# Kernel optimization log

Hardware: AMD Instinct MI355X
Metric: run time of the kernel (lower is better)

The kernel has to match this reference:

```python
import jax, jax.numpy as jnp
import numpy as np

B, S, H, D = 32, 127, 4, 64
HD = H * D
SCALE = 1.0 / np.sqrt(D).astype(np.float32)
NEG = -100000.0


def _remove_mask_keep(seq_len):
    # For q>=3, rows are grouped in 2-row blocks starting at i=3,5,...;
    # each block may only attend (among k>=3) to its own two columns.
    q = jnp.arange(seq_len)[:, None]
    k = jnp.arange(seq_len)[None, :]
    blk = 3 + 2 * ((q - 3) // 2)
    return (q < 3) | (k < 3) | ((k >= blk) & (k < blk + 2))  # [S, S] bool


def setup_inputs() -> dict:
    rng = jax.random.key(0)
    ks = jax.random.split(rng, 16)
    n = lambda k, shape: jax.random.normal(k, shape, dtype=jnp.float32)
    w = 1.0 / np.sqrt(HD).astype(np.float32)
    return {
        "query": n(ks[0], (B, S, HD)),
        "key": n(ks[1], (B, S, HD)),
        "value": n(ks[2], (B, S, HD)),
        "graph": jax.random.randint(ks[3], (B, S, S), 0, 2, dtype=jnp.int32),
        "edge_key": n(ks[4], (B, S, S, D)),
        "edge_value": n(ks[5], (B, S, S, D)),
        "edge_query": n(ks[6], (B, S, S, D)),
        "Wq": n(ks[7], (HD, HD)) * w, "bq": jnp.zeros((HD,), jnp.float32),
        "Wk": n(ks[8], (HD, HD)) * w, "bk": jnp.zeros((HD,), jnp.float32),
        "Wv": n(ks[9], (HD, HD)) * w, "bv": jnp.zeros((HD,), jnp.float32),
        "Wo": n(ks[10], (HD, HD)) * w, "bo": jnp.zeros((HD,), jnp.float32),
    }


def reference(query, key, value, graph, edge_key, edge_value, edge_query,
              Wq, bq, Wk, bk, Wv, bv, Wo, bo):
    b, s, _ = query.shape
    q = (query @ Wq.T + bq).reshape(b, s, H, D)
    k = (key @ Wk.T + bk).reshape(b, s, H, D)
    v = (value @ Wv.T + bv).reshape(b, s, H, D)

    scores = (
        jnp.einsum('bqhd,bkhd->bhqk', q, k)
        + jnp.einsum('bqhd,bqkd->bhqk', q, edge_key)
        + jnp.einsum('bkqd,bkhd->bhqk', edge_query, k)
        + jnp.einsum('bkqd,bqkd->bqk', edge_query, edge_key)[:, None]
    ) * SCALE

    mask = (graph != 0)[:, None, :, :] & _remove_mask_keep(s)[None, None]
    scores = jnp.where(mask, scores, NEG)
    attn = jax.nn.softmax(scores, axis=-1)  # dropout p=0 -> identity

    x = (jnp.einsum('bhqk,bkhd->bqhd', attn, v)
         + jnp.einsum('bhqk,bqkd->bqhd', attn, edge_value)).reshape(b, s, HD)
    return x @ Wo.T + bo
```

## Files before the change

### kernel.cpp

```cpp
#include <hip/hip_runtime.h>
#include <hip/hip_bf16.h>

#define S_LEN 127
#define NB    32
#define HDIM  256
#define DH    64
#define SCALE_F 0.125f

typedef __bf16 bf16x8 __attribute__((ext_vector_type(8)));
typedef __bf16 bf16x4 __attribute__((ext_vector_type(4)));
typedef float  f32x4  __attribute__((ext_vector_type(4)));

#define NTOK  4064
#define NW4   16384

__device__ __forceinline__ float4 b2f4(bf16x4 v) {
  return make_float4((float)v[0], (float)v[1], (float)v[2], (float)v[3]);
}

__global__ __launch_bounds__(256) void convert_w(
    const float* __restrict__ Wq, const float* __restrict__ Wk,
    const float* __restrict__ Wv, const float* __restrict__ Wo,
    __bf16* __restrict__ Wqb, __bf16* __restrict__ Wkb,
    __bf16* __restrict__ Wvb, __bf16* __restrict__ Wob)
{
  size_t t = (size_t)blockIdx.x * 256 + threadIdx.x;
  const float* src; __bf16* dst;
  if (t < NW4)                 { src = Wq; dst = Wqb; }
  else if ((t -= NW4) < NW4)   { src = Wk; dst = Wkb; }
  else if ((t -= NW4) < NW4)   { src = Wv; dst = Wvb; }
  else { t -= NW4;               src = Wo; dst = Wob; }
  const float4 x = ((const float4*)src)[t];
  bf16x4 r;
  r[0] = (__bf16)x.x; r[1] = (__bf16)x.y; r[2] = (__bf16)x.z; r[3] = (__bf16)x.w;
  ((bf16x4*)dst)[t] = r;
}

__global__ __launch_bounds__(256) void gemm_qkv(
    const float* __restrict__ q_in, const float* __restrict__ k_in,
    const float* __restrict__ v_in,
    const __bf16* __restrict__ Wqb, const float* __restrict__ bq,
    const __bf16* __restrict__ Wkb, const float* __restrict__ bk,
    const __bf16* __restrict__ Wvb, const float* __restrict__ bv,
    __bf16* __restrict__ qpb, __bf16* __restrict__ kpb, __bf16* __restrict__ vpb)
{
  const int tile = blockIdx.x;
  const float* A; const __bf16* W; const float* bias; __bf16* o;
  if (blockIdx.y == 0)      { A = q_in; W = Wqb; bias = bq; o = qpb; }
  else if (blockIdx.y == 1) { A = k_in; W = Wkb; bias = bk; o = kpb; }
  else                      { A = v_in; W = Wvb; bias = bv; o = vpb; }

  __shared__ __bf16 sA[32][264];
  const int row0 = tile * 32;

#pragma unroll
  for (int j = 0; j < 8; ++j) {
    const int f = threadIdx.x + j * 256;
    const int rr = f >> 6, c4 = f & 63;
    const float4 x = *(const float4*)(A + (size_t)(row0 + rr) * HDIM + c4 * 4);
    __bf16* d = &sA[rr][c4 * 4];
    d[0] = (__bf16)x.x; d[1] = (__bf16)x.y; d[2] = (__bf16)x.z; d[3] = (__bf16)x.w;
  }
  __syncthreads();

  const int w    = threadIdx.x >> 6;
  const int lane = threadIdx.x & 63;
  const int r    = lane & 15;
  const int ksl  = (lane >> 4) << 3;
  const int wc   = w * 64;

  const __bf16* Wb = W + (size_t)(wc + r) * HDIM + ksl;
  f32x4 acc[2][4] = {};

  bf16x8 cw[4];
#pragma unroll
  for (int ni = 0; ni < 4; ++ni)
    cw[ni] = *(const bf16x8*)(Wb + (size_t)ni * 16 * HDIM);
#pragma unroll
  for (int kb = 0; kb < 8; ++kb) {
    bf16x8 nw[4];
    if (kb < 7) {
#pragma unroll
      for (int ni = 0; ni < 4; ++ni)
        nw[ni] = *(const bf16x8*)(Wb + (size_t)ni * 16 * HDIM + (kb + 1) * 32);
    }
    const bf16x8 a0 = *(const bf16x8*)&sA[r][kb * 32 + ksl];
    const bf16x8 a1 = *(const bf16x8*)&sA[16 + r][kb * 32 + ksl];
#pragma unroll
    for (int ni = 0; ni < 4; ++ni) {
      acc[0][ni] = __builtin_amdgcn_mfma_f32_16x16x32_bf16(a0, cw[ni], acc[0][ni], 0, 0, 0);
      acc[1][ni] = __builtin_amdgcn_mfma_f32_16x16x32_bf16(a1, cw[ni], acc[1][ni], 0, 0, 0);
    }
    if (kb < 7) {
#pragma unroll
      for (int ni = 0; ni < 4; ++ni) cw[ni] = nw[ni];
    }
  }
  const int crow = (lane >> 4) * 4;
  const int ccol = lane & 15;
#pragma unroll
  for (int mi = 0; mi < 2; ++mi)
#pragma unroll
    for (int ni = 0; ni < 4; ++ni) {
      const int oc = wc + ni * 16 + ccol;
      const float bv = bias[oc];
#pragma unroll
      for (int rg = 0; rg < 4; ++rg)
        o[(size_t)(row0 + mi * 16 + crow + rg) * HDIM + oc] =
            (__bf16)(acc[mi][ni][rg] + bv);
    }
}

__global__ __launch_bounds__(256) void gemm_o(
    const __bf16* __restrict__ A, const __bf16* __restrict__ W,
    const float* __restrict__ bias, float* __restrict__ out)
{
  const int w = threadIdx.x >> 6;
  const int tile = blockIdx.x * 4 + w;
  if (tile >= 127) return;
  const int row0 = tile * 32, col0 = blockIdx.y * 32;
  const int lane = threadIdx.x & 63;
  const int r  = lane & 15;
  const int ks = (lane >> 4) << 3;
  const __bf16* Ab = A + (size_t)(row0 + r) * HDIM + ks;
  const __bf16* Wb = W + (size_t)(col0 + r) * HDIM + ks;
  f32x4 acc[2][2] = {};

  bf16x8 ca[2], cw[2];
  ca[0] = *(const bf16x8*)Ab;
  ca[1] = *(const bf16x8*)(Ab + (size_t)16 * HDIM);
  cw[0] = *(const bf16x8*)Wb;
  cw[1] = *(const bf16x8*)(Wb + (size_t)16 * HDIM);
#pragma unroll
  for (int kb = 0; kb < 8; ++kb) {
    bf16x8 na[2], nw[2];
    if (kb < 7) {
      const int off = (kb + 1) * 32;
      na[0] = *(const bf16x8*)(Ab + off);
      na[1] = *(const bf16x8*)(Ab + (size_t)16 * HDIM + off);
      nw[0] = *(const bf16x8*)(Wb + off);
      nw[1] = *(const bf16x8*)(Wb + (size_t)16 * HDIM + off);
    }
#pragma unroll
    for (int mi = 0; mi < 2; ++mi)
#pragma unroll
      for (int ni = 0; ni < 2; ++ni)
        acc[mi][ni] = __builtin_amdgcn_mfma_f32_16x16x32_bf16(
            ca[mi], cw[ni], acc[mi][ni], 0, 0, 0);
    if (kb < 7) {
      ca[0] = na[0]; ca[1] = na[1];
      cw[0] = nw[0]; cw[1] = nw[1];
    }
  }
  const int crow = (lane >> 4) * 4;
  const int ccol = lane & 15;
#pragma unroll
  for (int mi = 0; mi < 2; ++mi)
#pragma unroll
    for (int ni = 0; ni < 2; ++ni) {
      const int oc = col0 + ni * 16 + ccol;
      const float bv = bias[oc];
#pragma unroll
      for (int rg = 0; rg < 4; ++rg)
        out[(size_t)(row0 + mi * 16 + crow + rg) * HDIM + oc] = acc[mi][ni][rg] + bv;
    }
}

__global__ __launch_bounds__(256) void attn_kernel(
    const __bf16* __restrict__ qpb, const __bf16* __restrict__ kpb,
    const __bf16* __restrict__ vpb, const int* __restrict__ graph,
    const float* __restrict__ ekt, const float* __restrict__ evt,
    const float* __restrict__ eqt, __bf16* __restrict__ xpb)
{
  int b, q;
  {
    const int bx = blockIdx.x;
    if (bx < 96) { b = bx / 3; q = bx % 3; }
    else { const int rr = bx - 96; b = rr / 124; q = 3 + rr % 124; }
  }
  const int t = threadIdx.x;
  const int w = t >> 6;
  const int l = t & 63;
  const int ll = l & 15;
  const int g  = l >> 4;

  __shared__ int   s_list[S_LEN];
  __shared__ float s_attn[4][S_LEN];
  __shared__ int   s_cnt[2];

  bool valid = false;
  const int k0 = w * 64 + l;
  if (w < 2 && k0 < S_LEN) {
    const int gr = graph[((size_t)b * S_LEN + q) * S_LEN + k0];
    bool keep;
    if (q < 3 || k0 < 3) keep = true;
    else {
      const int blk = 3 + 2 * ((q - 3) >> 1);
      keep = (k0 >= blk) & (k0 < blk + 2);
    }
    valid = (gr != 0) && keep;
  }
  const unsigned long long bal = __ballot(valid);
  if (w < 2 && l == 0) s_cnt[w] = (int)__popcll(bal);
  __syncthreads();
  int n = s_cnt[0] + s_cnt[1];
  if (valid) {
    const int pos = (int)__popcll(bal & ((1ull << l) - 1ull)) + (w ? s_cnt[0] : 0);
    s_list[pos] = k0;
  }
  __syncthreads();

  if (n == 0) {
    if (t < S_LEN) {
      s_list[t] = t;
      const float u = 1.0f / 127.0f;
      s_attn[0][t] = u; s_attn[1][t] = u; s_attn[2][t] = u; s_attn[3][t] = u;
    }
    n = S_LEN;
  } else {
    const __bf16* qrow = qpb + ((size_t)b * S_LEN + q) * HDIM;
    float4 q4[4];
#pragma unroll
    for (int h = 0; h < 4; ++h)
      q4[h] = b2f4(*(const bf16x4*)(qrow + h * 64 + ll * 4));
    const float* eqb2 = eqt + ((size_t)b * S_LEN * S_LEN + q) * DH;
    const float* ekb2 = ekt + ((size_t)(b * S_LEN + q)) * S_LEN * DH;
    const __bf16* kpbb = kpb + (size_t)b * S_LEN * HDIM;
    const int myi = w * 4 + g;

    float4 ceq, cek;
    bf16x4 ck0, ck1, ck2, ck3;
    if (myi < n) {
      const int kk = s_list[myi];
      ceq = *(const float4*)(eqb2 + (size_t)kk * (S_LEN * DH) + ll * 4);
      cek = *(const float4*)(ekb2 + kk * DH + ll * 4);
      const __bf16* kr = kpbb + (size_t)kk * HDIM + ll * 4;
      ck0 = *(const bf16x4*)(kr);
      ck1 = *(const bf16x4*)(kr + 64);
      ck2 = *(const bf16x4*)(kr + 128);
      ck3 = *(const bf16x4*)(kr + 192);
    }
    for (int i0 = 0; i0 < n; i0 += 16) {
      const int i = i0 + myi;
      float4 neq, nek;
      bf16x4 nk0, nk1, nk2, nk3;
      const int j = i + 16;
      if (j < n) {
        const int kk = s_list[j];
        neq = *(const float4*)(eqb2 + (size_t)kk * (S_LEN * DH) + ll * 4);
        nek = *(const float4*)(ekb2 + kk * DH + ll * 4);
        const __bf16* kr = kpbb + (size_t)kk * HDIM + ll * 4;
        nk0 = *(const bf16x4*)(kr);
        nk1 = *(const bf16x4*)(kr + 64);
        nk2 = *(const bf16x4*)(kr + 128);
        nk3 = *(const bf16x4*)(kr + 192);
      }
      float p0 = 0.f, p1 = 0.f, p2 = 0.f, p3 = 0.f;
      if (i < n) {
        const float4 k0f = b2f4(ck0), k1f = b2f4(ck1),
                     k2f = b2f4(ck2), k3f = b2f4(ck3);
        p0 = (q4[0].x+ceq.x)*(k0f.x+cek.x) + (q4[0].y+ceq.y)*(k0f.y+cek.y)
           + (q4[0].z+ceq.z)*(k0f.z+cek.z) + (q4[0].w+ceq.w)*(k0f.w+cek.w);
        p1 = (q4[1].x+ceq.x)*(k1f.x+cek.x) + (q4[1].y+ceq.y)*(k1f.y+cek.y)
           + (q4[1].z+ceq.z)*(k1f.z+cek.z) + (q4[1].w+ceq.w)*(k1f.w+cek.w);
        p2 = (q4[2].x+ceq.x)*(k2f.x+cek.x) + (q4[2].y+ceq.y)*(k2f.y+cek.y)
           + (q4[2].z+ceq.z)*(k2f.z+cek.z) + (q4[2].w+ceq.w)*(k2f.w+cek.w);
        p3 = (q4[3].x+ceq.x)*(k3f.x+cek.x) + (q4[3].y+ceq.y)*(k3f.y+cek.y)
           + (q4[3].z+ceq.z)*(k3f.z+cek.z) + (q4[3].w+ceq.w)*(k3f.w+cek.w);
      }
#pragma unroll
      for (int off = 1; off < 16; off <<= 1) {
        p0 += __shfl_xor(p0, off, 64);
        p1 += __shfl_xor(p1, off, 64);
        p2 += __shfl_xor(p2, off, 64);
        p3 += __shfl_xor(p3, off, 64);
      }
      if (i < n && ll < 4) {
        const float s = (ll == 0) ? p0 : (ll == 1) ? p1 : (ll == 2) ? p2 : p3;
        s_attn[ll][i] = s * SCALE_F;
      }
      ceq = neq; cek = nek;
      ck0 = nk0; ck1 = nk1; ck2 = nk2; ck3 = nk3;
    }
    __syncthreads();

    {
      const float v0 = (l < n) ? s_attn[w][l] : -INFINITY;
      const float v1 = (64 + l < n) ? s_attn[w][64 + l] : -INFINITY;
      float mx = fmaxf(v0, v1);
#pragma unroll
      for (int off = 32; off; off >>= 1) mx = fmaxf(mx, __shfl_xor(mx, off, 64));
      const float e0 = (l < n) ? expf(v0 - mx) : 0.f;
      const float e1 = (64 + l < n) ? expf(v1 - mx) : 0.f;
      float sm = e0 + e1;
#pragma unroll
      for (int off = 32; off; off >>= 1) sm += __shfl_xor(sm, off, 64);
      const float inv = 1.0f / sm;
      if (l < n) s_attn[w][l] = e0 * inv;
      if (64 + l < n) s_attn[w][64 + l] = e1 * inv;
    }
  }
  __syncthreads();

  {
    const float* evb2 = evt + ((size_t)(b * S_LEN + q)) * S_LEN * DH;
    const __bf16* vbp = vpb + (size_t)b * S_LEN * HDIM + w * DH + ll * 4;
    float ax = 0.f, ay = 0.f, az = 0.f, aw2 = 0.f;

    int i = g;
    float a = 0.f; bf16x4 v4; float4 e4;
    if (i < n) {
      const int kk = s_list[i];
      a = s_attn[w][i];
      v4 = *(const bf16x4*)(vbp + (size_t)kk * HDIM);
      e4 = *(const float4*)(evb2 + kk * DH + ll * 4);
    }
    while (i < n) {
      const int j = i + 4;
      float a2 = 0.f; bf16x4 v42; float4 e42;
      if (j < n) {
        const int kk = s_list[j];
        a2 = s_attn[w][j];
        v42 = *(const bf16x4*)(vbp + (size_t)kk * HDIM);
        e42 = *(const float4*)(evb2 + kk * DH + ll * 4);
      }
      const float4 vf = b2f4(v4);
      ax  += a * (vf.x + e4.x);
      ay  += a * (vf.y + e4.y);
      az  += a * (vf.z + e4.z);
      aw2 += a * (vf.w + e4.w);
      i = j; a = a2; v4 = v42; e4 = e42;
    }
#pragma unroll
    for (int off = 16; off < 64; off <<= 1) {
      ax  += __shfl_xor(ax, off, 64);
      ay  += __shfl_xor(ay, off, 64);
      az  += __shfl_xor(az, off, 64);
      aw2 += __shfl_xor(aw2, off, 64);
    }
    if (g == 0) {
      bf16x4 rr;
      rr[0] = (__bf16)ax; rr[1] = (__bf16)ay;
      rr[2] = (__bf16)az; rr[3] = (__bf16)aw2;
      *(bf16x4*)(xpb + ((size_t)b * S_LEN + q) * HDIM + w * 64 + ll * 4) = rr;
    }
  }
}

extern "C" void kernel_launch(void* const* d_in, const int* in_sizes, int n_in,
                              void* d_out, int out_size, void* d_ws, size_t ws_size,
                              hipStream_t stream) {
  const float* query = (const float*)d_in[0];
  const float* key   = (const float*)d_in[1];
  const float* value = (const float*)d_in[2];
  const int*   graph = (const int*)d_in[3];
  const float* ekt   = (const float*)d_in[4];
  const float* evt   = (const float*)d_in[5];
  const float* eqt   = (const float*)d_in[6];
  const float* Wq = (const float*)d_in[7];  const float* bq = (const float*)d_in[8];
  const float* Wk = (const float*)d_in[9];  const float* bk = (const float*)d_in[10];
  const float* Wv = (const float*)d_in[11]; const float* bv = (const float*)d_in[12];
  const float* Wo = (const float*)d_in[13]; const float* bo = (const float*)d_in[14];
  float* out = (float*)d_out;

  const size_t NE = (size_t)NTOK * HDIM;
  char* p = (char*)d_ws;
  __bf16* qpb = (__bf16*)p;         p += NE * 2;
  __bf16* kpb = (__bf16*)p;         p += NE * 2;
  __bf16* vpb = (__bf16*)p;         p += NE * 2;
  __bf16* xpb = (__bf16*)p;         p += NE * 2;
  __bf16* Wqb = (__bf16*)p;         p += (size_t)HDIM * HDIM * 2;
  __bf16* Wkb = (__bf16*)p;         p += (size_t)HDIM * HDIM * 2;
  __bf16* Wvb = (__bf16*)p;         p += (size_t)HDIM * HDIM * 2;
  __bf16* Wob = (__bf16*)p;

  convert_w<<<dim3(256), 256, 0, stream>>>(Wq, Wk, Wv, Wo, Wqb, Wkb, Wvb, Wob);
  gemm_qkv<<<dim3(127, 3), 256, 0, stream>>>(query, key, value,
                                             Wqb, bq, Wkb, bk, Wvb, bv,
                                             qpb, kpb, vpb);
  attn_kernel<<<dim3(NB * S_LEN), 256, 0, stream>>>(qpb, kpb, vpb, graph,
                                                    ekt, evt, eqt, xpb);
  gemm_o<<<dim3(32, 8), 256, 0, stream>>>(xpb, Wob, bo, out);
}
```

Baseline: 51.99 us.

## Fuse output projection into attention kernel with 4 tokens per block

Merges the attention kernel and the output-projection GEMM into one kernel. Each 1024-thread block handles four (batch, query) items, keeps their attention outputs in LDS, and multiplies them by Wo with MFMA, padding the 16-row tile with zeros. This drops the separate gemm_o launch and the global round trip of the intermediate x tensor. In exchange, every block rereads the whole 256x256 Wo, only 4 of 16 MFMA rows are useful, and the larger blocks with more barriers can lower occupancy.

After: 84.91 us. 63.3% more time.

```diff
diff --git a/kernel.cpp b/kernel.cpp
--- a/kernel.cpp
+++ b/kernel.cpp
@@ -111,82 +111,37 @@
     }
 }
 
-__global__ __launch_bounds__(256) void gemm_o(
-    const __bf16* __restrict__ A, const __bf16* __restrict__ W,
-    const float* __restrict__ bias, float* __restrict__ out)
-{
-  const int w = threadIdx.x >> 6;
-  const int tile = blockIdx.x * 4 + w;
-  if (tile >= 127) return;
-  const int row0 = tile * 32, col0 = blockIdx.y * 32;
-  const int lane = threadIdx.x & 63;
-  const int r  = lane & 15;
-  const int ks = (lane >> 4) << 3;
-  const __bf16* Ab = A + (size_t)(row0 + r) * HDIM + ks;
-  const __bf16* Wb = W + (size_t)(col0 + r) * HDIM + ks;
-  f32x4 acc[2][2] = {};
-
-  bf16x8 ca[2], cw[2];
-  ca[0] = *(const bf16x8*)Ab;
-  ca[1] = *(const bf16x8*)(Ab + (size_t)16 * HDIM);
-  cw[0] = *(const bf16x8*)Wb;
-  cw[1] = *(const bf16x8*)(Wb + (size_t)16 * HDIM);
-#pragma unroll
-  for (int kb = 0; kb < 8; ++kb) {
-    bf16x8 na[2], nw[2];
-    if (kb < 7) {
-      const int off = (kb + 1) * 32;
-      na[0] = *(const bf16x8*)(Ab + off);
-      na[1] = *(const bf16x8*)(Ab + (size_t)16 * HDIM + off);
-      nw[0] = *(const bf16x8*)(Wb + off);
-      nw[1] = *(const bf16x8*)(Wb + (size_t)16 * HDIM + off);
-    }
-#pragma unroll
-    for (int mi = 0; mi < 2; ++mi)
-#pragma unroll
-      for (int ni = 0; ni < 2; ++ni)
-        acc[mi][ni] = __builtin_amdgcn_mfma_f32_16x16x32_bf16(
-            ca[mi], cw[ni], acc[mi][ni], 0, 0, 0);
-    if (kb < 7) {
-      ca[0] = na[0]; ca[1] = na[1];
-      cw[0] = nw[0]; cw[1] = nw[1];
-    }
-  }
-  const int crow = (lane >> 4) * 4;
-  const int ccol = lane & 15;
-#pragma unroll
-  for (int mi = 0; mi < 2; ++mi)
-#pragma unroll
-    for (int ni = 0; ni < 2; ++ni) {
-      const int oc = col0 + ni * 16 + ccol;
-      const float bv = bias[oc];
-#pragma unroll
-      for (int rg = 0; rg < 4; ++rg)
-        out[(size_t)(row0 + mi * 16 + crow + rg) * HDIM + oc] = acc[mi][ni][rg] + bv;
-    }
-}
-
-__global__ __launch_bounds__(256) void attn_kernel(
+__global__ __launch_bounds__(1024) void attn_o(
     const __bf16* __restrict__ qpb, const __bf16* __restrict__ kpb,
     const __bf16* __restrict__ vpb, const int* __restrict__ graph,
     const float* __restrict__ ekt, const float* __restrict__ evt,
-    const float* __restrict__ eqt, __bf16* __restrict__ xpb)
+    const float* __restrict__ eqt,
+    const __bf16* __restrict__ Wob, const float* __restrict__ bo,
+    float* __restrict__ out)
 {
-  int b, q;
-  {
-    const int bx = blockIdx.x;
-    if (bx < 96) { b = bx / 3; q = bx % 3; }
-    else { const int rr = bx - 96; b = rr / 124; q = 3 + rr % 124; }
-  }
-  const int t = threadIdx.x;
-  const int w = t >> 6;
-  const int l = t & 63;
+  const int s  = threadIdx.x >> 8;
+  const int t  = threadIdx.x & 255;
+  const int w  = t >> 6;
+  const int l  = t & 63;
   const int ll = l & 15;
   const int g  = l >> 4;
 
-  __shared__ int   s_list[S_LEN];
-  __shared__ float s_attn[4][S_LEN];
-  __shared__ int   s_cnt[2];
+  __shared__ int    s_list[4][S_LEN];
+  __shared__ float  s_attn[4][4][S_LEN];
+  __shared__ int    s_cnt[4][2];
+  __shared__ int    s_tok[4];
+  __shared__ __bf16 x_lds[16][264];
+
+  for (int z = threadIdx.x; z < 12 * 264; z += 1024) {
+    const int zr = z / 264;
+    x_lds[4 + zr][z - zr * 264] = (__bf16)0.f;
+  }
+
+  const int item = blockIdx.x + s * 1016;
+  int b, q;
+  if (item < 96) { b = item / 3; q = item % 3; }
+  else { const int rr = item - 96; b = rr / 124; q = 3 + rr % 124; }
+  if (t == 0) s_tok[s] = b * S_LEN + q;
 
   bool valid = false;
   const int k0 = w * 64 + l;
@@ -201,20 +156,22 @@
     valid = (gr != 0) && keep;
   }
   const unsigned long long bal = __ballot(valid);
-  if (w < 2 && l == 0) s_cnt[w] = (int)__popcll(bal);
-  __syncthreads();
-  int n = s_cnt[0] + s_cnt[1];
+  if (w < 2 && l == 0) s_cnt[s][w] = (int)__popcll(bal);
+  __syncthreads();
+  int n = s_cnt[s][0] + s_cnt[s][1];
   if (valid) {
-    const int pos = (int)__popcll(bal & ((1ull << l) - 1ull)) + (w ? s_cnt[0] : 0);
-    s_list[pos] = k0;
-  }
-  __syncthreads();
-
-  if (n == 0) {
+    const int pos = (int)__popcll(bal & ((1ull << l) - 1ull)) + (w ? s_cnt[s][0] : 0);
+    s_list[s][pos] = k0;
+  }
+  __syncthreads();
+
+  const bool uni = (n == 0);
+  if (uni) {
     if (t < S_LEN) {
-      s_list[t] = t;
+      s_list[s][t] = t;
       const float u = 1.0f / 127.0f;
-      s_attn[0][t] = u; s_attn[1][t] = u; s_attn[2][t] = u; s_attn[3][t] = u;
+      s_attn[s][0][t] = u; s_attn[s][1][t] = u;
+      s_attn[s][2][t] = u; s_attn[s][3][t] = u;
     }
     n = S_LEN;
   } else {
@@ -231,7 +188,7 @@
     float4 ceq, cek;
     bf16x4 ck0, ck1, ck2, ck3;
     if (myi < n) {
-      const int kk = s_list[myi];
+      const int kk = s_list[s][myi];
       ceq = *(const float4*)(eqb2 + (size_t)kk * (S_LEN * DH) + ll * 4);
       cek = *(const float4*)(ekb2 + kk * DH + ll * 4);
       const __bf16* kr = kpbb + (size_t)kk * HDIM + ll * 4;
@@ -246,7 +203,7 @@
       bf16x4 nk0, nk1, nk2, nk3;
       const int j = i + 16;
       if (j < n) {
-        const int kk = s_list[j];
+        const int kk = s_list[s][j];
         neq = *(const float4*)(eqb2 + (size_t)kk * (S_LEN * DH) + ll * 4);
         nek = *(const float4*)(ekb2 + kk * DH + ll * 4);
         const __bf16* kr = kpbb + (size_t)kk * HDIM + ll * 4;
@@ -276,29 +233,29 @@
         p3 += __shfl_xor(p3, off, 64);
       }
       if (i < n && ll < 4) {
-        const float s = (ll == 0) ? p0 : (ll == 1) ? p1 : (ll == 2) ? p2 : p3;
-        s_attn[ll][i] = s * SCALE_F;
+        const float sc = (ll == 0) ? p0 : (ll == 1) ? p1 : (ll == 2) ? p2 : p3;
+        s_attn[s][ll][i] = sc * SCALE_F;
       }
       ceq = neq; cek = nek;
       ck0 = nk0; ck1 = nk1; ck2 = nk2; ck3 = nk3;
     }
-    __syncthreads();
-
-    {
-      const float v0 = (l < n) ? s_attn[w][l] : -INFINITY;
-      const float v1 = (64 + l < n) ? s_attn[w][64 + l] : -INFINITY;
-      float mx = fmaxf(v0, v1);
-#pragma unroll
-      for (int off = 32; off; off >>= 1) mx = fmaxf(mx, __shfl_xor(mx, off, 64));
-      const float e0 = (l < n) ? expf(v0 - mx) : 0.f;
-      const float e1 = (64 + l < n) ? expf(v1 - mx) : 0.f;
-      float sm = e0 + e1;
-#pragma unroll
-      for (int off = 32; off; off >>= 1) sm += __shfl_xor(sm, off, 64);
-      const float inv = 1.0f / sm;
-      if (l < n) s_attn[w][l] = e0 * inv;
-      if (64 + l < n) s_attn[w][64 + l] = e1 * inv;
-    }
+  }
+  __syncthreads();
+
+  if (!uni) {
+    const float v0 = (l < n) ? s_attn[s][w][l] : -INFINITY;
+    const float v1 = (64 + l < n) ? s_attn[s][w][64 + l] : -INFINITY;
+    float mx = fmaxf(v0, v1);
+#pragma unroll
+    for (int off = 32; off; off >>= 1) mx = fmaxf(mx, __shfl_xor(mx, off, 64));
+    const float e0 = (l < n) ? expf(v0 - mx) : 0.f;
+    const float e1 = (64 + l < n) ? expf(v1 - mx) : 0.f;
+    float sm = e0 + e1;
+#pragma unroll
+    for (int off = 32; off; off >>= 1) sm += __shfl_xor(sm, off, 64);
+    const float inv = 1.0f / sm;
+    if (l < n) s_attn[s][w][l] = e0 * inv;
+    if (64 + l < n) s_attn[s][w][64 + l] = e1 * inv;
   }
   __syncthreads();
 
@@ -310,8 +267,8 @@
     int i = g;
     float a = 0.f; bf16x4 v4; float4 e4;
     if (i < n) {
-      const int kk = s_list[i];
-      a = s_attn[w][i];
+      const int kk = s_list[s][i];
+      a = s_attn[s][w][i];
       v4 = *(const bf16x4*)(vbp + (size_t)kk * HDIM);
       e4 = *(const float4*)(evb2 + kk * DH + ll * 4);
     }
@@ -319,8 +276,8 @@
       const int j = i + 4;
       float a2 = 0.f; bf16x4 v42; float4 e42;
       if (j < n) {
-        const int kk = s_list[j];
-        a2 = s_attn[w][j];
+        const int kk = s_list[s][j];
+        a2 = s_attn[s][w][j];
         v42 = *(const bf16x4*)(vbp + (size_t)kk * HDIM);
         e42 = *(const float4*)(evb2 + kk * DH + ll * 4);
       }
@@ -342,7 +299,33 @@
       bf16x4 rr;
       rr[0] = (__bf16)ax; rr[1] = (__bf16)ay;
       rr[2] = (__bf16)az; rr[3] = (__bf16)aw2;
-      *(bf16x4*)(xpb + ((size_t)b * S_LEN + q) * HDIM + w * 64 + ll * 4) = rr;
+      *(bf16x4*)&x_lds[s][w * 64 + ll * 4] = rr;
+    }
+  }
+  __syncthreads();
+
+  {
+    const int wav  = threadIdx.x >> 6;
+    const int lane = threadIdx.x & 63;
+    const int r    = lane & 15;
+    const int ks   = (lane >> 4) << 3;
+    const int c0   = wav * 16;
+    const __bf16* Wb = Wob + (size_t)(c0 + r) * HDIM + ks;
+    f32x4 acc = {};
+    bf16x8 cw = *(const bf16x8*)Wb;
+#pragma unroll
+    for (int kb = 0; kb < 8; ++kb) {
+      bf16x8 nw;
+      if (kb < 7) nw = *(const bf16x8*)(Wb + (kb + 1) * 32);
+      const bf16x8 a = *(const bf16x8*)&x_lds[r][kb * 32 + ks];
+      acc = __builtin_amdgcn_mfma_f32_16x16x32_bf16(a, cw, acc, 0, 0, 0);
+      if (kb < 7) cw = nw;
+    }
+    if ((lane >> 4) == 0) {
+      const float bv = bo[c0 + r];
+#pragma unroll
+      for (int rg = 0; rg < 4; ++rg)
+        out[(size_t)s_tok[rg] * HDIM + c0 + r] = acc[rg] + bv;
     }
   }
 }
@@ -368,7 +351,6 @@
   __bf16* qpb = (__bf16*)p;         p += NE * 2;
   __bf16* kpb = (__bf16*)p;         p += NE * 2;
   __bf16* vpb = (__bf16*)p;         p += NE * 2;
-  __bf16* xpb = (__bf16*)p;         p += NE * 2;
   __bf16* Wqb = (__bf16*)p;         p += (size_t)HDIM * HDIM * 2;
   __bf16* Wkb = (__bf16*)p;         p += (size_t)HDIM * HDIM * 2;
   __bf16* Wvb = (__bf16*)p;         p += (size_t)HDIM * HDIM * 2;
@@ -378,7 +360,6 @@
   gemm_qkv<<<dim3(127, 3), 256, 0, stream>>>(query, key, value,
                                              Wqb, bq, Wkb, bk, Wvb, bv,
                                              qpb, kpb, vpb);
-  attn_kernel<<<dim3(NB * S_LEN), 256, 0, stream>>>(qpb, kpb, vpb, graph,
-                                                    ekt, evt, eqt, xpb);
-  gemm_o<<<dim3(32, 8), 256, 0, stream>>>(xpb, Wob, bo, out);
-}
+  attn_o<<<dim3(1016), 1024, 0, stream>>>(qpb, kpb, vpb, graph,
+                                          ekt, evt, eqt, Wob, bo, out);
+}
```

## Split attention into dense-row blocks and one-wave-per-row sparse path

Applied to the files above, without the earlier changes.

Replaces the one-block-per-query-row attention kernel with a kernel that keeps dense 256-thread blocks for the first three query rows but packs four sparse rows (q>=3) per block, one wave each. In the sparse path each wave handles only its five possible key columns directly, computing scores, softmax and weighted value sums in registers with a small shared buffer. This cuts the grid from 4064 to 1088 blocks and drops the ballot/compaction and most block-wide barriers. In exchange the dense rows now process all keys with NEG masking instead of a compacted list, which changes masked-row behaviour slightly.

Result: slower. 56.58 us (+8.8%).

```diff
diff --git a/kernel.cpp b/kernel.cpp
--- a/kernel.cpp
+++ b/kernel.cpp
@@ -6,6 +6,7 @@
 #define HDIM  256
 #define DH    64
 #define SCALE_F 0.125f
+#define NEG_F  -100000.0f
 
 typedef __bf16 bf16x8 __attribute__((ext_vector_type(8)));
 typedef __bf16 bf16x4 __attribute__((ext_vector_type(4)));
@@ -111,6 +112,234 @@
     }
 }
 
+__global__ __launch_bounds__(256) void attn_x(
+    const __bf16* __restrict__ qpb, const __bf16* __restrict__ kpb,
+    const __bf16* __restrict__ vpb, const int* __restrict__ graph,
+    const float* __restrict__ ekt, const float* __restrict__ evt,
+    const float* __restrict__ eqt, __bf16* __restrict__ xpb)
+{
+  const int w  = threadIdx.x >> 6;
+  const int l  = threadIdx.x & 63;
+  const int ll = l & 15;
+  const int g  = l >> 4;
+
+  __shared__ float s_attn[4][S_LEN];
+  __shared__ float s_mskf[S_LEN];
+  __shared__ float s_sc[4][4][5];
+
+  if (blockIdx.x < 96) {
+    const int b = blockIdx.x / 3, q = blockIdx.x % 3;
+
+    if (w < 2) {
+      const int k0 = w * 64 + l;
+      if (k0 < S_LEN)
+        s_mskf[k0] = (graph[((size_t)b * S_LEN + q) * S_LEN + k0] != 0) ? 1.f : 0.f;
+    }
+    __syncthreads();
+
+    const __bf16* qrow = qpb + ((size_t)b * S_LEN + q) * HDIM;
+    float4 q4[4];
+#pragma unroll
+    for (int h = 0; h < 4; ++h)
+      q4[h] = b2f4(*(const bf16x4*)(qrow + h * 64 + ll * 4));
+    const float* eqb2 = eqt + ((size_t)b * S_LEN * S_LEN + q) * DH;
+    const float* ekb2 = ekt + ((size_t)(b * S_LEN + q)) * S_LEN * DH;
+    const __bf16* kpbb = kpb + (size_t)b * S_LEN * HDIM;
+
+    for (int i0 = 0; i0 < S_LEN; i0 += 16) {
+      const int i = i0 + w * 4 + g;
+      float p0 = 0.f, p1 = 0.f, p2 = 0.f, p3 = 0.f;
+      if (i < S_LEN) {
+        const float4 eq4 = *(const float4*)(eqb2 + (size_t)i * (S_LEN * DH) + ll * 4);
+        const float4 ek4 = *(const float4*)(ekb2 + (size_t)i * DH + ll * 4);
+        const __bf16* kr = kpbb + (size_t)i * HDIM + ll * 4;
+        const float4 k0f = b2f4(*(const bf16x4*)(kr));
+        const float4 k1f = b2f4(*(const bf16x4*)(kr + 64));
+        const float4 k2f = b2f4(*(const bf16x4*)(kr + 128));
+        const float4 k3f = b2f4(*(const bf16x4*)(kr + 192));
+        p0 = (q4[0].x+eq4.x)*(k0f.x+ek4.x) + (q4[0].y+eq4.y)*(k0f.y+ek4.y)
+           + (q4[0].z+eq4.z)*(k0f.z+ek4.z) + (q4[0].w+eq4.w)*(k0f.w+ek4.w);
+        p1 = (q4[1].x+eq4.x)*(k1f.x+ek4.x) + (q4[1].y+eq4.y)*(k1f.y+ek4.y)
+           + (q4[1].z+eq4.z)*(k1f.z+ek4.z) + (q4[1].w+eq4.w)*(k1f.w+ek4.w);
+        p2 = (q4[2].x+eq4.x)*(k2f.x+ek4.x) + (q4[2].y+eq4.y)*(k2f.y+ek4.y)
+           + (q4[2].z+eq4.z)*(k2f.z+ek4.z) + (q4[2].w+eq4.w)*(k2f.w+ek4.w);
+        p3 = (q4[3].x+eq4.x)*(k3f.x+ek4.x) + (q4[3].y+eq4.y)*(k3f.y+ek4.y)
+           + (q4[3].z+eq4.z)*(k3f.z+ek4.z) + (q4[3].w+eq4.w)*(k3f.w+ek4.w);
+      }
+#pragma unroll
+      for (int off = 1; off < 16; off <<= 1) {
+        p0 += __shfl_xor(p0, off, 64);
+        p1 += __shfl_xor(p1, off, 64);
+        p2 += __shfl_xor(p2, off, 64);
+        p3 += __shfl_xor(p3, off, 64);
+      }
+      if (i < S_LEN && ll < 4) {
+        const float sc = (ll == 0) ? p0 : (ll == 1) ? p1 : (ll == 2) ? p2 : p3;
+        s_attn[ll][i] = (s_mskf[i] != 0.f) ? sc * SCALE_F : NEG_F;
+      }
+    }
+    __syncthreads();
+
+    {
+      const float v0 = (l < S_LEN) ? s_attn[w][l] : -INFINITY;
+      const float v1 = (64 + l < S_LEN) ? s_attn[w][64 + l] : -INFINITY;
+      float mx = fmaxf(v0, v1);
+#pragma unroll
+      for (int off = 32; off; off >>= 1) mx = fmaxf(mx, __shfl_xor(mx, off, 64));
+      const float e0 = (l < S_LEN) ? expf(v0 - mx) : 0.f;
+      const float e1 = (64 + l < S_LEN) ? expf(v1 - mx) : 0.f;
+      float sm = e0 + e1;
+#pragma unroll
+      for (int off = 32; off; off >>= 1) sm += __shfl_xor(sm, off, 64);
+      const float inv = 1.0f / sm;
+      if (l < S_LEN) s_attn[w][l] = e0 * inv;
+      if (64 + l < S_LEN) s_attn[w][64 + l] = e1 * inv;
+    }
+    __syncthreads();
+
+    {
+      const float* evb2 = evt + ((size_t)(b * S_LEN + q)) * S_LEN * DH;
+      const __bf16* vbp = vpb + (size_t)b * S_LEN * HDIM + w * DH + ll * 4;
+      float ax = 0.f, ay = 0.f, az = 0.f, aw2 = 0.f;
+#pragma unroll 4
+      for (int i = g; i < S_LEN; i += 4) {
+        const float a = s_attn[w][i];
+        const float4 vf = b2f4(*(const bf16x4*)(vbp + (size_t)i * HDIM));
+        const float4 e4 = *(const float4*)(evb2 + (size_t)i * DH + ll * 4);
+        ax  += a * (vf.x + e4.x);
+        ay  += a * (vf.y + e4.y);
+        az  += a * (vf.z + e4.z);
+        aw2 += a * (vf.w + e4.w);
+      }
+#pragma unroll
+      for (int off = 16; off < 64; off <<= 1) {
+        ax  += __shfl_xor(ax, off, 64);
+        ay  += __shfl_xor(ay, off, 64);
+        az  += __shfl_xor(az, off, 64);
+        aw2 += __shfl_xor(aw2, off, 64);
+      }
+      if (g == 0) {
+        bf16x4 rr;
+        rr[0] = (__bf16)ax; rr[1] = (__bf16)ay;
+        rr[2] = (__bf16)az; rr[3] = (__bf16)aw2;
+        *(bf16x4*)(xpb + ((size_t)b * S_LEN + q) * HDIM + w * 64 + ll * 4) = rr;
+      }
+    }
+  } else {
+    const int widx = (blockIdx.x - 96) * 4 + w;
+    const int b = widx / 124;
+    const int q = 3 + widx % 124;
+    const int blk = 3 + 2 * ((q - 3) >> 1);
+
+    bool gb = false;
+    if (l < 5) {
+      const int c = (l < 3) ? l : blk + (l - 3);
+      gb = graph[((size_t)b * S_LEN + q) * S_LEN + c] != 0;
+    }
+    const unsigned mask5 = (unsigned)(__ballot(gb) & 31ull);
+
+    if (mask5) {
+      const __bf16* qrow = qpb + ((size_t)b * S_LEN + q) * HDIM;
+      float4 q4[4];
+#pragma unroll
+      for (int h = 0; h < 4; ++h)
+        q4[h] = b2f4(*(const bf16x4*)(qrow + h * 64 + ll * 4));
+      const float* eqb2 = eqt + ((size_t)b * S_LEN * S_LEN + q) * DH;
+      const float* ekb2 = ekt + ((size_t)(b * S_LEN + q)) * S_LEN * DH;
+      const __bf16* kpbb = kpb + (size_t)b * S_LEN * HDIM;
+
+#pragma unroll
+      for (int it = 0; it < 2; ++it) {
+        const bool act = (it == 0) || (g == 0);
+        const int ci = (it == 0) ? g : 4;
+        const int c = (ci < 3) ? ci : blk + (ci - 3);
+        float p0 = 0.f, p1 = 0.f, p2 = 0.f, p3 = 0.f;
+        if (act) {
+          const float4 eq4 = *(const float4*)(eqb2 + (size_t)c * (S_LEN * DH) + ll * 4);
+          const float4 ek4 = *(const float4*)(ekb2 + (size_t)c * DH + ll * 4);
+          const __bf16* kr = kpbb + (size_t)c * HDIM + ll * 4;
+          const float4 k0f = b2f4(*(const bf16x4*)(kr));
+          const float4 k1f = b2f4(*(const bf16x4*)(kr + 64));
+          const float4 k2f = b2f4(*(const bf16x4*)(kr + 128));
+          const float4 k3f = b2f4(*(const bf16x4*)(kr + 192));
+          p0 = (q4[0].x+eq4.x)*(k0f.x+ek4.x) + (q4[0].y+eq4.y)*(k0f.y+ek4.y)
+             + (q4[0].z+eq4.z)*(k0f.z+ek4.z) + (q4[0].w+eq4.w)*(k0f.w+ek4.w);
+          p1 = (q4[1].x+eq4.x)*(k1f.x+ek4.x) + (q4[1].y+eq4.y)*(k1f.y+ek4.y)
+             + (q4[1].z+eq4.z)*(k1f.z+ek4.z) + (q4[1].w+eq4.w)*(k1f.w+ek4.w);
+          p2 = (q4[2].x+eq4.x)*(k2f.x+ek4.x) + (q4[2].y+eq4.y)*(k2f.y+ek4.y)
+             + (q4[2].z+eq4.z)*(k2f.z+ek4.z) + (q4[2].w+eq4.w)*(k2f.w+ek4.w);
+          p3 = (q4[3].x+eq4.x)*(k3f.x+ek4.x) + (q4[3].y+eq4.y)*(k3f.y+ek4.y)
+             + (q4[3].z+eq4.z)*(k3f.z+ek4.z) + (q4[3].w+eq4.w)*(k3f.w+ek4.w);
+        }
+#pragma unroll
+        for (int off = 1; off < 16; off <<= 1) {
+          p0 += __shfl_xor(p0, off, 64);
+          p1 += __shfl_xor(p1, off, 64);
+          p2 += __shfl_xor(p2, off, 64);
+          p3 += __shfl_xor(p3, off, 64);
+        }
+        if (act && ll < 4) {
+          const float sc = (ll == 0) ? p0 : (ll == 1) ? p1 : (ll == 2) ? p2 : p3;
+          s_sc[w][ll][ci] = ((mask5 >> ci) & 1) ? sc * SCALE_F : NEG_F;
+        }
+      }
+    }
+    __syncthreads();
+
+    float acc0 = 0.f, acc1 = 0.f, acc2 = 0.f, acc3 = 0.f;
+    const float* evb2 = evt + ((size_t)(b * S_LEN + q)) * S_LEN * DH;
+    const __bf16* vrow_base = vpb + (size_t)b * S_LEN * HDIM;
+
+    if (mask5) {
+      float wgt[4][5];
+#pragma unroll
+      for (int h = 0; h < 4; ++h) {
+        float m = -INFINITY;
+#pragma unroll
+        for (int ci = 0; ci < 5; ++ci) m = fmaxf(m, s_sc[w][h][ci]);
+        float sum = 0.f;
+#pragma unroll
+        for (int ci = 0; ci < 5; ++ci) {
+          const float e = expf(s_sc[w][h][ci] - m);
+          wgt[h][ci] = e; sum += e;
+        }
+        const float inv = 1.0f / sum;
+#pragma unroll
+        for (int ci = 0; ci < 5; ++ci) wgt[h][ci] *= inv;
+      }
+#pragma unroll
+      for (int ci = 0; ci < 5; ++ci) {
+        if (!((mask5 >> ci) & 1)) continue;
+        const int c = (ci < 3) ? ci : blk + (ci - 3);
+        const float ev = evb2[(size_t)c * DH + l];
+        const __bf16* vr = vrow_base + (size_t)c * HDIM;
+        acc0 += wgt[0][ci] * ((float)vr[l]       + ev);
+        acc1 += wgt[1][ci] * ((float)vr[64 + l]  + ev);
+        acc2 += wgt[2][ci] * ((float)vr[128 + l] + ev);
+        acc3 += wgt[3][ci] * ((float)vr[192 + l] + ev);
+      }
+    } else {
+#pragma unroll 4
+      for (int c = 0; c < S_LEN; ++c) {
+        const float ev = evb2[(size_t)c * DH + l];
+        const __bf16* vr = vrow_base + (size_t)c * HDIM;
+        acc0 += (float)vr[l]       + ev;
+        acc1 += (float)vr[64 + l]  + ev;
+        acc2 += (float)vr[128 + l] + ev;
+        acc3 += (float)vr[192 + l] + ev;
+      }
+      const float u = 1.0f / 127.0f;
+      acc0 *= u; acc1 *= u; acc2 *= u; acc3 *= u;
+    }
+
+    __bf16* xr = xpb + ((size_t)b * S_LEN + q) * HDIM;
+    xr[l]       = (__bf16)acc0;
+    xr[64 + l]  = (__bf16)acc1;
+    xr[128 + l] = (__bf16)acc2;
+    xr[192 + l] = (__bf16)acc3;
+  }
+}
+
 __global__ __launch_bounds__(256) void gemm_o(
     const __bf16* __restrict__ A, const __bf16* __restrict__ W,
     const float* __restrict__ bias, float* __restrict__ out)
@@ -164,187 +393,6 @@
       for (int rg = 0; rg < 4; ++rg)
         out[(size_t)(row0 + mi * 16 + crow + rg) * HDIM + oc] = acc[mi][ni][rg] + bv;
     }
-}
-
-__global__ __launch_bounds__(256) void attn_kernel(
-    const __bf16* __restrict__ qpb, const __bf16* __restrict__ kpb,
-    const __bf16* __restrict__ vpb, const int* __restrict__ graph,
-    const float* __restrict__ ekt, const float* __restrict__ evt,
-    const float* __restrict__ eqt, __bf16* __restrict__ xpb)
-{
-  int b, q;
-  {
-    const int bx = blockIdx.x;
-    if (bx < 96) { b = bx / 3; q = bx % 3; }
-    else { const int rr = bx - 96; b = rr / 124; q = 3 + rr % 124; }
-  }
-  const int t = threadIdx.x;
-  const int w = t >> 6;
-  const int l = t & 63;
-  const int ll = l & 15;
-  const int g  = l >> 4;
-
-  __shared__ int   s_list[S_LEN];
-  __shared__ float s_attn[4][S_LEN];
-  __shared__ int   s_cnt[2];
-
-  bool valid = false;
-  const int k0 = w * 64 + l;
-  if (w < 2 && k0 < S_LEN) {
-    const int gr = graph[((size_t)b * S_LEN + q) * S_LEN + k0];
-    bool keep;
-    if (q < 3 || k0 < 3) keep = true;
-    else {
-      const int blk = 3 + 2 * ((q - 3) >> 1);
-      keep = (k0 >= blk) & (k0 < blk + 2);
-    }
-    valid = (gr != 0) && keep;
-  }
-  const unsigned long long bal = __ballot(valid);
-  if (w < 2 && l == 0) s_cnt[w] = (int)__popcll(bal);
-  __syncthreads();
-  int n = s_cnt[0] + s_cnt[1];
-  if (valid) {
-    const int pos = (int)__popcll(bal & ((1ull << l) - 1ull)) + (w ? s_cnt[0] : 0);
-    s_list[pos] = k0;
-  }
-  __syncthreads();
-
-  if (n == 0) {
-    if (t < S_LEN) {
-      s_list[t] = t;
-      const float u = 1.0f / 127.0f;
-      s_attn[0][t] = u; s_attn[1][t] = u; s_attn[2][t] = u; s_attn[3][t] = u;
-    }
-    n = S_LEN;
-  } else {
-    const __bf16* qrow = qpb + ((size_t)b * S_LEN + q) * HDIM;
-    float4 q4[4];
-#pragma unroll
-    for (int h = 0; h < 4; ++h)
-      q4[h] = b2f4(*(const bf16x4*)(qrow + h * 64 + ll * 4));
-    const float* eqb2 = eqt + ((size_t)b * S_LEN * S_LEN + q) * DH;
-    const float* ekb2 = ekt + ((size_t)(b * S_LEN + q)) * S_LEN * DH;
-    const __bf16* kpbb = kpb + (size_t)b * S_LEN * HDIM;
-    const int myi = w * 4 + g;
-
-    float4 ceq, cek;
-    bf16x4 ck0, ck1, ck2, ck3;
-    if (myi < n) {
-      const int kk = s_list[myi];
-      ceq = *(const float4*)(eqb2 + (size_t)kk * (S_LEN * DH) + ll * 4);
-      cek = *(const float4*)(ekb2 + kk * DH + ll * 4);
-      const __bf16* kr = kpbb + (size_t)kk * HDIM + ll * 4;
-      ck0 = *(const bf16x4*)(kr);
-      ck1 = *(const bf16x4*)(kr + 64);
-      ck2 = *(const bf16x4*)(kr + 128);
-      ck3 = *(const bf16x4*)(kr + 192);
-    }
-    for (int i0 = 0; i0 < n; i0 += 16) {
-      const int i = i0 + myi;
-      float4 neq, nek;
-      bf16x4 nk0, nk1, nk2, nk3;
-      const int j = i + 16;
-      if (j < n) {
-        const int kk = s_list[j];
-        neq = *(const float4*)(eqb2 + (size_t)kk * (S_LEN * DH) + ll * 4);
-        nek = *(const float4*)(ekb2 + kk * DH + ll * 4);
-        const __bf16* kr = kpbb + (size_t)kk * HDIM + ll * 4;
-        nk0 = *(const bf16x4*)(kr);
-        nk1 = *(const bf16x4*)(kr + 64);
-        nk2 = *(const bf16x4*)(kr + 128);
-        nk3 = *(const bf16x4*)(kr + 192);
-      }
-      float p0 = 0.f, p1 = 0.f, p2 = 0.f, p3 = 0.f;
-      if (i < n) {
-        const float4 k0f = b2f4(ck0), k1f = b2f4(ck1),
-                     k2f = b2f4(ck2), k3f = b2f4(ck3);
-        p0 = (q4[0].x+ceq.x)*(k0f.x+cek.x) + (q4[0].y+ceq.y)*(k0f.y+cek.y)
-           + (q4[0].z+ceq.z)*(k0f.z+cek.z) + (q4[0].w+ceq.w)*(k0f.w+cek.w);
-        p1 = (q4[1].x+ceq.x)*(k1f.x+cek.x) + (q4[1].y+ceq.y)*(k1f.y+cek.y)
-           + (q4[1].z+ceq.z)*(k1f.z+cek.z) + (q4[1].w+ceq.w)*(k1f.w+cek.w);
-        p2 = (q4[2].x+ceq.x)*(k2f.x+cek.x) + (q4[2].y+ceq.y)*(k2f.y+cek.y)
-           + (q4[2].z+ceq.z)*(k2f.z+cek.z) + (q4[2].w+ceq.w)*(k2f.w+cek.w);
-        p3 = (q4[3].x+ceq.x)*(k3f.x+cek.x) + (q4[3].y+ceq.y)*(k3f.y+cek.y)
-           + (q4[3].z+ceq.z)*(k3f.z+cek.z) + (q4[3].w+ceq.w)*(k3f.w+cek.w);
-      }
-#pragma unroll
-      for (int off = 1; off < 16; off <<= 1) {
-        p0 += __shfl_xor(p0, off, 64);
-        p1 += __shfl_xor(p1, off, 64);
-        p2 += __shfl_xor(p2, off, 64);
-        p3 += __shfl_xor(p3, off, 64);
-      }
-      if (i < n && ll < 4) {
-        const float s = (ll == 0) ? p0 : (ll == 1) ? p1 : (ll == 2) ? p2 : p3;
-        s_attn[ll][i] = s * SCALE_F;
-      }
-      ceq = neq; cek = nek;
-      ck0 = nk0; ck1 = nk1; ck2 = nk2; ck3 = nk3;
-    }
-    __syncthreads();
-
-    {
-      const float v0 = (l < n) ? s_attn[w][l] : -INFINITY;
-      const float v1 = (64 + l < n) ? s_attn[w][64 + l] : -INFINITY;
-      float mx = fmaxf(v0, v1);
-#pragma unroll
-      for (int off = 32; off; off >>= 1) mx = fmaxf(mx, __shfl_xor(mx, off, 64));
-      const float e0 = (l < n) ? expf(v0 - mx) : 0.f;
-      const float e1 = (64 + l < n) ? expf(v1 - mx) : 0.f;
-      float sm = e0 + e1;
-#pragma unroll
-      for (int off = 32; off; off >>= 1) sm += __shfl_xor(sm, off, 64);
-      const float inv = 1.0f / sm;
-      if (l < n) s_attn[w][l] = e0 * inv;
-      if (64 + l < n) s_attn[w][64 + l] = e1 * inv;
-    }
-  }
-  __syncthreads();
-
-  {
-    const float* evb2 = evt + ((size_t)(b * S_LEN + q)) * S_LEN * DH;
-    const __bf16* vbp = vpb + (size_t)b * S_LEN * HDIM + w * DH + ll * 4;
-    float ax = 0.f, ay = 0.f, az = 0.f, aw2 = 0.f;
-
-    int i = g;
-    float a = 0.f; bf16x4 v4; float4 e4;
-    if (i < n) {
-      const int kk = s_list[i];
-      a = s_attn[w][i];
-      v4 = *(const bf16x4*)(vbp + (size_t)kk * HDIM);
-      e4 = *(const float4*)(evb2 + kk * DH + ll * 4);
-    }
-    while (i < n) {
-      const int j = i + 4;
-      float a2 = 0.f; bf16x4 v42; float4 e42;
-      if (j < n) {
-        const int kk = s_list[j];
-        a2 = s_attn[w][j];
-        v42 = *(const bf16x4*)(vbp + (size_t)kk * HDIM);
-        e42 = *(const float4*)(evb2 + kk * DH + ll * 4);
-      }
-      const float4 vf = b2f4(v4);
-      ax  += a * (vf.x + e4.x);
-      ay  += a * (vf.y + e4.y);
-      az  += a * (vf.z + e4.z);
-      aw2 += a * (vf.w + e4.w);
-      i = j; a = a2; v4 = v42; e4 = e42;
-    }
-#pragma unroll
-    for (int off = 16; off < 64; off <<= 1) {
-      ax  += __shfl_xor(ax, off, 64);
-      ay  += __shfl_xor(ay, off, 64);
-      az  += __shfl_xor(az, off, 64);
-      aw2 += __shfl_xor(aw2, off, 64);
-    }
-    if (g == 0) {
-      bf16x4 rr;
-      rr[0] = (__bf16)ax; rr[1] = (__bf16)ay;
-      rr[2] = (__bf16)az; rr[3] = (__bf16)aw2;
-      *(bf16x4*)(xpb + ((size_t)b * S_LEN + q) * HDIM + w * 64 + ll * 4) = rr;
-    }
-  }
 }
 
 extern "C" void kernel_launch(void* const* d_in, const int* in_sizes, int n_in,
@@ -378,7 +426,7 @@
   gemm_qkv<<<dim3(127, 3), 256, 0, stream>>>(query, key, value,
                                              Wqb, bq, Wkb, bk, Wvb, bv,
                                              qpb, kpb, vpb);
-  attn_kernel<<<dim3(NB * S_LEN), 256, 0, stream>>>(qpb, kpb, vpb, graph,
-                                                    ekt, evt, eqt, xpb);
+  attn_x<<<dim3(96 + 992), 256, 0, stream>>>(qpb, kpb, vpb, graph,
+                                             ekt, evt, eqt, xpb);
   gemm_o<<<dim3(32, 8), 256, 0, stream>>>(xpb, Wob, bo, out);
 }
```
